# Kernel optimization log

Measured on AMD Instinct MI355X. Metric: run time of the kernel, lower is better.

The kernel has to match this reference:

```python
import jax, jax.numpy as jnp
import numpy as np

B, K, N, D, H, NNEG, NTOP = 8, 8, 128, 256, 128, 64, 64
UNARY_SCALES = (1.0, 1.0, 1.0)  # one scale per tree level, tree_height = log2(K) = 3


def setup_inputs():
    key = jax.random.key(0)
    ks = jax.random.split(key, 8)
    s = 0.05
    return {
        'pos_fea': jax.random.normal(ks[0], (B, K, N, D), jnp.float32),
        'neg_fea': jax.random.normal(ks[1], (B * K, NNEG, D), jnp.float32),
        'pos_classes': jax.random.randint(ks[2], (B, K, N), 0, 20),
        'target_class': jax.random.randint(ks[3], (B,), 0, 20),
        'Wp1': jax.random.normal(ks[4], (2 * D, H), jnp.float32) * s,
        'bp1': jnp.zeros((H,), jnp.float32),
        'Wp2': jax.random.normal(ks[5], (H, 1), jnp.float32) * s,
        'bp2': jnp.zeros((1,), jnp.float32),
        'Wu1': jax.random.normal(ks[6], (2 * D, H), jnp.float32) * s,
        'bu1': jnp.zeros((H,), jnp.float32),
        'Wu2': jax.random.normal(ks[7], (H, 1), jnp.float32) * s,
        'bu2': jnp.zeros((1,), jnp.float32),
    }


def _relation(f0, f1, W1, b1, W2, b2):
    # RelationModule: Dense(H, relu) -> Dense(1) applied to concat([f0_m, f1_n])
    # for every cross pair; concat-Dense is split into two GEMMs. -> [Bn, M0, M1]
    d = f0.shape[-1]
    h0 = jnp.einsum('bmd,dh->bmh', f0, W1[:d])
    h1 = jnp.einsum('bnd,dh->bnh', f1, W1[d:])
    h = jax.nn.relu(h0[:, :, None, :] + h1[:, None, :, :] + b1)
    return jnp.einsum('bmnh,h->bmn', h, W2[:, 0]) + b2[0]


def _bg(t, idx):
    # batched_gather along axis 1: t [Bn, P, ...], idx [Bn, T]
    ie = idx.reshape(idx.shape + (1,) * (t.ndim - 2))
    ie = jnp.broadcast_to(ie, idx.shape + t.shape[2:])
    return jnp.take_along_axis(t, ie, axis=1)


def _rep(fea, sub):
    # subproblem representative feature: fea [Bn,S,N,D], sub [Bn,M,S] -> [Bn,M,D]
    idx = jnp.swapaxes(sub, 1, 2)[..., None]              # [Bn,S,M,1]
    idx = jnp.broadcast_to(idx, idx.shape[:-1] + (fea.shape[-1],))
    return jnp.take_along_axis(fea, idx, axis=2).mean(axis=1)


def _tree(pos_fea, neg_fea, Wp1, bp1, Wp2, bp2, Wu1, bu1, Wu2, bu2):
    pos_flat = pos_fea.reshape(B * K, N, D)
    # UnaryModule: mean relation score of each positive proposal vs the negative bag
    ue = _relation(pos_flat, neg_fea, Wu1, bu1, Wu2, bu2).mean(-1)   # [B*K, N]
    sub = jnp.broadcast_to(jnp.arange(N, dtype=jnp.int32)[None, :, None], (B * K, N, 1))
    pe = jnp.zeros_like(ue)
    tree_height = int(np.log2(K))
    best = None
    for i in range(tree_height):
        S = 2 ** i                      # subproblem size per branch at this level
        Bn = sub.shape[0] // 2
        M = sub.shape[1]
        sub2 = sub.reshape(Bn, 2, M, S)  # [::2] / [1::2] split of adjacent rows
        sub0, sub1 = sub2[:, 0], sub2[:, 1]
        pe2 = pe.reshape(Bn, 2, M)
        ue2 = ue.reshape(Bn, 2, M)
        fea = pos_flat.reshape(Bn, 2, S, N, D)
        rep0 = _rep(fea[:, 0], sub0)
        rep1 = _rep(fea[:, 1], sub1)
        # PairwiseCrossSimilarity: scores for all cross pairs of candidates
        scores = _relation(rep0, rep1, Wp1, bp1, Wp2, bp2).reshape(Bn, M * M)
        p0 = jnp.repeat(jnp.arange(M), M)
        p1 = jnp.tile(jnp.arange(M), M)
        pe = pe2[:, 0][:, p0] + pe2[:, 1][:, p1] - scores
        ue = ue2[:, 0][:, p0] + ue2[:, 1][:, p1]
        total = pe + UNARY_SCALES[i] * ue
        sub = jnp.concatenate([sub0[:, p0], sub1[:, p1]], axis=-1)  # [Bn, M*M, 2S]
        topk = 1 if i == tree_height - 1 else min(M * M, NTOP)
        _, inds = jax.lax.top_k(-total, topk)
        sub = _bg(sub, inds)
        ue = jnp.take_along_axis(ue, inds, axis=1)
        pe = jnp.take_along_axis(pe, inds, axis=1)
        best = jnp.take_along_axis(total, inds, axis=1)
    return sub, best


def reference(pos_fea, neg_fea, pos_classes, target_class,
              Wp1, bp1, Wp2, bp2, Wu1, bu1, Wu2, bu2):
    sub, _ = _tree(pos_fea, neg_fea, Wp1, bp1, Wp2, bp2, Wu1, bu1, Wu2, bu2)
    is_target = (pos_classes == target_class[:, None, None]).astype(jnp.float32)
    return sub[:, 0], is_target  # selected proposal per image [B,K], [B,K,N]
```

## Files before the change

### kernel.cpp

```cpp
#include <hip/hip_runtime.h>
#include <stdint.h>

#define B_ 8
#define K_ 8
#define N_ 128
#define D_ 256
#define H_ 128
#define NNEG_ 64

typedef unsigned long long u64;
typedef float f4 __attribute__((ext_vector_type(4)));

__device__ __forceinline__ u64 shfl_xor_u64(u64 v, int m) {
    int lo = __shfl_xor((int)(unsigned)v, m, 64);
    int hi = __shfl_xor((int)(unsigned)(v >> 32), m, 64);
    return ((u64)(unsigned)hi << 32) | (unsigned)lo;
}
__device__ __forceinline__ u64 bitonic_merge64(u64 m, int lane) {
#pragma unroll
    for (int j = 32; j > 0; j >>= 1) {
        u64 o = shfl_xor_u64(m, j);
        bool keepMin = ((lane & j) == 0);
        bool lt = m < o;
        m = (keepMin == lt) ? m : o;
    }
    return m;
}
__device__ __forceinline__ u64 merge2(u64 a, u64 b, int lane) {
    u64 br = shfl_xor_u64(b, 63);
    u64 m = a < br ? a : br;
    return bitonic_merge64(m, lane);
}
__device__ __forceinline__ unsigned sortable(float f) {
    unsigned u = __float_as_uint(f);
    return (u & 0x80000000u) ? ~u : (u | 0x80000000u);
}
__device__ __forceinline__ float unsortable(unsigned u) {
    return __uint_as_float((u & 0x80000000u) ? (u & 0x7FFFFFFFu) : ~u);
}
__device__ __forceinline__ void sort128_reg(u64& v0, u64& v1, int lane) {
#pragma unroll
    for (int k = 2; k <= 64; k <<= 1) {
        bool d0 = ((lane & k) == 0);
        bool d1 = (k == 64) ? false : d0;
#pragma unroll
        for (int j = k >> 1; j > 0; j >>= 1) {
            u64 o0 = shfl_xor_u64(v0, j);
            bool km0 = (((lane & j) == 0) == d0);
            v0 = (km0 == (v0 < o0)) ? v0 : o0;
            u64 o1 = shfl_xor_u64(v1, j);
            bool km1 = (((lane & j) == 0) == d1);
            v1 = (km1 == (v1 < o1)) ? v1 : o1;
        }
    }
    if (v0 > v1) { u64 tmp = v0; v0 = v1; v1 = tmp; }
#pragma unroll
    for (int j = 32; j > 0; j >>= 1) {
        bool km = ((lane & j) == 0);
        u64 o0 = shfl_xor_u64(v0, j);
        v0 = (km == (v0 < o0)) ? v0 : o0;
        u64 o1 = shfl_xor_u64(v1, j);
        v1 = (km == (v1 < o1)) ? v1 : o1;
    }
}

__global__ __launch_bounds__(128) void g1_gemm(
    const float* __restrict__ pos, const float* __restrict__ neg,
    const float* __restrict__ Wu1, const float* __restrict__ Wp1,
    const int* __restrict__ pos_classes, const int* __restrict__ target_class,
    float* __restrict__ HU0, float* __restrict__ HU1n,
    float* __restrict__ HP0, float* __restrict__ HP1,
    float* __restrict__ outp) {
    int bid = blockIdx.x;
    int t = threadIdx.x;
    if (bid >= 896) {
        int base = (bid - 896) * 2048 + t * 16;
#pragma unroll
        for (int q = 0; q < 16; ++q) {
            int idx = base + q;
            outp[64 + idx] = (pos_classes[idx] == target_class[idx >> 10]) ? 1.0f : 0.0f;
        }
        return;
    }
    const float* A; const float* W; float* OUT; int bid2;
    if (bid < 256)      { A = pos; W = Wu1;           OUT = HU0;  bid2 = bid; }
    else if (bid < 384) { A = neg; W = Wu1 + D_ * H_; OUT = HU1n; bid2 = bid - 256; }
    else if (bid < 640) { A = pos; W = Wp1;           OUT = HP0;  bid2 = bid - 384; }
    else                { A = pos; W = Wp1 + D_ * H_; OUT = HP1;  bid2 = bid - 640; }
    int rb = (bid2 >> 1) * 64;
    int cb64 = (bid2 & 1) * 64;

    __shared__ float As[2][64][36];
    int tx = t & 7, ty = t >> 3;
    f4 acc[4][2];
#pragma unroll
    for (int i = 0; i < 4; ++i) { acc[i][0] = (f4)0.f; acc[i][1] = (f4)0.f; }

    const float* Wb = W + cb64 + tx * 8;

#pragma unroll
    for (int rep = 0; rep < 4; ++rep) {
        int flat = t + rep * 128;
        int row = flat >> 3, kq = flat & 7;
        *(f4*)&As[0][row][kq * 4] = *(const f4*)&A[(size_t)(rb + row) * D_ + kq * 4];
    }
    f4 bcur[4][2], bnxt[4][2];
#pragma unroll
    for (int q = 0; q < 4; ++q) {
        bcur[q][0] = *(const f4*)&Wb[(size_t)q * H_];
        bcur[q][1] = *(const f4*)&Wb[(size_t)q * H_ + 4];
    }
    __syncthreads();

    for (int chunk = 0; chunk < 8; ++chunk) {
        int cur = chunk & 1, nxt = cur ^ 1;
        bool pre = (chunk < 7);
        f4 pa[4];
        if (pre) {
            int k0n = (chunk + 1) * 32;
#pragma unroll
            for (int rep = 0; rep < 4; ++rep) {
                int flat = t + rep * 128;
                int row = flat >> 3, kq = flat & 7;
                pa[rep] = *(const f4*)&A[(size_t)(rb + row) * D_ + k0n + kq * 4];
            }
        }
#pragma unroll
        for (int g = 0; g < 8; ++g) {
            int kg = chunk * 8 + g;
            if (kg + 1 < 64) {
                int kb = (kg + 1) * 4;
#pragma unroll
                for (int q = 0; q < 4; ++q) {
                    bnxt[q][0] = *(const f4*)&Wb[(size_t)(kb + q) * H_];
                    bnxt[q][1] = *(const f4*)&Wb[(size_t)(kb + q) * H_ + 4];
                }
            }
            f4 av[4];
#pragma unroll
            for (int i = 0; i < 4; ++i)
                av[i] = *(const f4*)&As[cur][ty * 4 + i][g * 4];
#pragma unroll
            for (int q = 0; q < 4; ++q) {
                f4 b0 = bcur[q][0], b1 = bcur[q][1];
#pragma unroll
                for (int i = 0; i < 4; ++i) {
                    float a = av[i][q];
                    acc[i][0][0] += a * b0[0]; acc[i][0][1] += a * b0[1];
                    acc[i][0][2] += a * b0[2]; acc[i][0][3] += a * b0[3];
                    acc[i][1][0] += a * b1[0]; acc[i][1][1] += a * b1[1];
                    acc[i][1][2] += a * b1[2]; acc[i][1][3] += a * b1[3];
                }
            }
#pragma unroll
            for (int q = 0; q < 4; ++q) { bcur[q][0] = bnxt[q][0]; bcur[q][1] = bnxt[q][1]; }
        }
        if (pre) {
#pragma unroll
            for (int rep = 0; rep < 4; ++rep) {
                int flat = t + rep * 128;
                int row = flat >> 3, kq = flat & 7;
                *(f4*)&As[nxt][row][kq * 4] = pa[rep];
            }
        }
        __syncthreads();
    }
#pragma unroll
    for (int i = 0; i < 4; ++i) {
        *(f4*)&OUT[(size_t)(rb + ty * 4 + i) * H_ + cb64 + tx * 8] = acc[i][0];
        *(f4*)&OUT[(size_t)(rb + ty * 4 + i) * H_ + cb64 + tx * 8 + 4] = acc[i][1];
    }
}

__global__ __launch_bounds__(128) void g2_ue_sc0(
    const float* __restrict__ HU0, const float* __restrict__ HU1n,
    const float* __restrict__ bu1, const float* __restrict__ Wu2,
    const float* __restrict__ bu2v,
    const float* __restrict__ HP0, const float* __restrict__ HP1,
    const float* __restrict__ bp1, const float* __restrict__ Wp2,
    const float* __restrict__ bp2,
    float* __restrict__ t0, float* __restrict__ sc0) {
    __shared__ float LsT[128][36];
    __shared__ float RsT[128][68];
    __shared__ float wsv[128];
    __shared__ float red[32][33];

    int bid = blockIdx.x;
    int t = threadIdx.x;
    bool is_ue = bid < 256;

    const float* Lsrc; const float* Rsrc; const float* b1v; const float* W2;
    if (is_ue) {
        int bk = bid >> 2, mt = bid & 3;
        Lsrc = HU0 + (size_t)(bk * N_ + mt * 32) * H_;
        Rsrc = HU1n + (size_t)bk * NNEG_ * H_;
        b1v = bu1; W2 = Wu2;
    } else {
        int bid2 = bid - 256;
        int b = bid2 >> 3, m0t = (bid2 >> 1) & 3, m1t = bid2 & 1;
        Lsrc = HP0 + (size_t)b * 2 * N_ * H_ + m0t * 32 * H_;
        Rsrc = HP1 + (size_t)b * 2 * N_ * H_ + N_ * H_ + m1t * 64 * H_;
        b1v = bp1; W2 = Wp2;
    }
    for (int i = t; i < 32 * 32; i += 128) {
        int m = i & 31, hq = i >> 5;
        const f4 a = *(const f4*)&Lsrc[(size_t)m * H_ + hq * 4];
        const f4 b = *(const f4*)&b1v[hq * 4];
        LsT[hq * 4 + 0][m] = a[0] + b[0];
        LsT[hq * 4 + 1][m] = a[1] + b[1];
        LsT[hq * 4 + 2][m] = a[2] + b[2];
        LsT[hq * 4 + 3][m] = a[3] + b[3];
    }
    for (int i = t; i < 64 * 32; i += 128) {
        int n = i & 63, hq = i >> 6;
        const f4 a = *(const f4*)&Rsrc[(size_t)n * H_ + hq * 4];
        RsT[hq * 4 + 0][n] = a[0];
        RsT[hq * 4 + 1][n] = a[1];
        RsT[hq * 4 + 2][n] = a[2];
        RsT[hq * 4 + 3][n] = a[3];
    }
    wsv[t] = W2[t];
    __syncthreads();

    int tm = t & 7, tn = t >> 3;
    f4 acc[4];
#pragma unroll
    for (int i = 0; i < 4; ++i) acc[i] = (f4)0.f;
#pragma unroll 2
    for (int hg = 0; hg < 32; ++hg) {
        f4 wv = *(const f4*)&wsv[hg * 4];
        f4 lv[4], rv[4];
#pragma unroll
        for (int s = 0; s < 4; ++s) {
            lv[s] = *(const f4*)&LsT[hg * 4 + s][tm * 4];
            rv[s] = *(const f4*)&RsT[hg * 4 + s][tn * 4];
        }
#pragma unroll
        for (int s = 0; s < 4; ++s) {
            float w = wv[s];
#pragma unroll
            for (int i = 0; i < 4; ++i) {
                float l = lv[s][i];
                float v;
                v = l + rv[s][0]; v = v > 0.f ? v : 0.f; acc[i][0] += v * w;
                v = l + rv[s][1]; v = v > 0.f ? v : 0.f; acc[i][1] += v * w;
                v = l + rv[s][2]; v = v > 0.f ? v : 0.f; acc[i][2] += v * w;
                v = l + rv[s][3]; v = v > 0.f ? v : 0.f; acc[i][3] += v * w;
            }
        }
    }

    if (is_ue) {
        int bk = bid >> 2, mt = bid & 3;
#pragma unroll
        for (int i = 0; i < 4; ++i) {
            red[tm * 4 + i][tn * 2 + 0] = acc[i][0] + acc[i][1];
            red[tm * 4 + i][tn * 2 + 1] = acc[i][2] + acc[i][3];
        }
        __syncthreads();
        if (t < 32) {
            float s = 0.f;
            for (int q = 0; q < 32; ++q) s += red[t][q];
            t0[bk * N_ + mt * 32 + t] = s * (1.0f / NNEG_) + bu2v[0];
        }
    } else {
        int bid2 = bid - 256;
        int b = bid2 >> 3, m0t = (bid2 >> 1) & 3, m1t = bid2 & 1;
        float bp2v = bp2[0];
        float* orow = sc0 + (size_t)b * 16384;
#pragma unroll
        for (int i = 0; i < 4; ++i) {
            int m0 = m0t * 32 + tm * 4 + i;
            int m1 = m1t * 64 + tn * 4;
            f4 o = {acc[i][0] + bp2v, acc[i][1] + bp2v,
                    acc[i][2] + bp2v, acc[i][3] + bp2v};
            *(f4*)&orow[m0 * 128 + m1] = o;
        }
    }
}

__global__ __launch_bounds__(256) void g3a_top0(const float* __restrict__ sc0,
                                                const float* __restrict__ t0,
                                                u64* __restrict__ g3c) {
    int bid = blockIdx.x;
    int r = bid >> 3, c = bid & 7;
    int t = threadIdx.x, lane = t & 63, w = t >> 6;
    __shared__ float tt[256];
    __shared__ u64 cand[4][128];
    if (t < 256) tt[t] = t0[r * 256 + t];
    __syncthreads();
    const float* row = sc0 + (size_t)r * 16384 + c * 2048 + w * 512;
    unsigned sv[8];
#pragma unroll
    for (int j = 0; j < 8; ++j) {
        int li = j * 64 + lane;
        int idx = c * 2048 + w * 512 + li;
        float v = (tt[idx >> 7] + tt[128 + (idx & 127)]) - row[li];
        sv[j] = sortable(v);
    }
    unsigned T = 0u;
#pragma unroll
    for (int it = 0; it < 16; ++it) {
        int p = 30 - 2 * it;
        unsigned C1 = T | (1u << p), C2 = T | (2u << p), C3 = T | (3u << p);
        unsigned c1 = 0u, c2 = 0u, c3 = 0u;
#pragma unroll
        for (int j = 0; j < 8; ++j) {
            c1 += (unsigned)__popcll(__ballot(sv[j] < C1));
            c2 += (unsigned)__popcll(__ballot(sv[j] < C2));
            c3 += (unsigned)__popcll(__ballot(sv[j] < C3));
        }
        unsigned k = (c3 < 64u) ? 3u : (c2 < 64u) ? 2u : (c1 < 64u) ? 1u : 0u;
        T |= (k << p);
    }
    u64* my = cand[w];
    int base = 0;
#pragma unroll
    for (int j = 0; j < 8; ++j) {
        u64 mask = __ballot(sv[j] <= T);
        if (sv[j] <= T) {
            int pos = base + (int)__popcll(mask & ((1ull << lane) - 1ull));
            if (pos < 128) {
                int idx = c * 2048 + w * 512 + j * 64 + lane;
                my[pos] = ((u64)sv[j] << 32) | (unsigned)idx;
            }
        }
        base += (int)__popcll(mask);
    }
    int cc = base < 128 ? base : 128;
    u64 v0 = (lane < cc) ? my[lane] : ~0ull;
    u64 v1 = (64 + lane < cc) ? my[64 + lane] : ~0ull;
    sort128_reg(v0, v1, lane);
    my[lane] = v0;
    __syncthreads();
    if (w == 0) {
        u64 x0 = cand[0][lane], x1 = cand[1][lane];
        u64 x2 = cand[2][lane], x3 = cand[3][lane];
        u64 y0 = merge2(x0, x1, lane), y1 = merge2(x2, x3, lane);
        g3c[(size_t)bid * 64 + lane] = merge2(y0, y1, lane);
    }
}

__global__ __launch_bounds__(256) void g4a_s1(
    const float* __restrict__ HP0, const float* __restrict__ HP1,
    const u64* __restrict__ g3c, int* __restrict__ pA,
    const float* __restrict__ bp1, const float* __restrict__ Wp2,
    const float* __restrict__ bp2, u64* __restrict__ g4top) {
    int bid = blockIdx.x;
    int u = bid >> 3, mq = (bid >> 1) & 3, nh = bid & 1;
    int t = threadIdx.x, lane = t & 63, w = t >> 6;
    __shared__ float LsT[128][17];
    __shared__ float RsT[128][34];
    __shared__ float taL[64], taR[64];
    __shared__ int paL[64], paR[64];
    __shared__ float wsv[128];
    __shared__ u64 cand[4][64];
    if (w < 2) {
        const u64* Lp = g3c + (size_t)(2 * u + w) * 512;
        u64 x0 = Lp[lane], x1 = Lp[64 + lane], x2 = Lp[128 + lane], x3 = Lp[192 + lane];
        u64 x4 = Lp[256 + lane], x5 = Lp[320 + lane], x6 = Lp[384 + lane], x7 = Lp[448 + lane];
        u64 y0 = merge2(x0, x1, lane), y1 = merge2(x2, x3, lane);
        u64 y2 = merge2(x4, x5, lane), y3 = merge2(x6, x7, lane);
        u64 z0 = merge2(y0, y1, lane), z1 = merge2(y2, y3, lane);
        u64 f = merge2(z0, z1, lane);
        int idx = (int)(f & 0xFFFFFFFFull);
        int pk = ((idx >> 7) << 8) | (idx & 127);
        float tv = unsortable((unsigned)(f >> 32));
        if (w == 0) { taL[lane] = tv; paL[lane] = pk; }
        else        { taR[lane] = tv; paR[lane] = pk; }
    }
    if (t >= 128) wsv[t - 128] = Wp2[t - 128];
    float bp2v = bp2[0];
    __syncthreads();
    if ((bid & 7) == 0) {
        if (t < 64) pA[(2 * u) * 64 + t] = paL[t];
        else if (t < 128) pA[(2 * u + 1) * 64 + (t - 64)] = paR[t - 64];
    }
    for (int i = t; i < 16 * 128; i += 256) {
        int m = i >> 7, h = i & 127;
        int pk = paL[mq * 16 + m]; int a0 = pk >> 8, a1 = pk & 255;
        float s = HP0[(size_t)(4 * u) * 16384 + a0 * 128 + h]
                + HP0[(size_t)(4 * u + 1) * 16384 + a1 * 128 + h];
        LsT[h][m] = s * 0.5f + bp1[h];
    }
    for (int i = t; i < 32 * 128; i += 256) {
        int n = i >> 7, h = i & 127;
        int pk = paR[nh * 32 + n]; int c0 = pk >> 8, c1 = pk & 255;
        float s = HP1[(size_t)(4 * u + 2) * 16384 + c0 * 128 + h]
                + HP1[(size_t)(4 * u + 3) * 16384 + c1 * 128 + h];
        RsT[h][n] = s * 0.5f;
    }
    __syncthreads();
    int lm = w * 4 + (lane >> 4);
    int ln = lane & 15;
    float a0 = 0.f, a1 = 0.f;
#pragma unroll 4
    for (int h = 0; h < 128; ++h) {
        float lv = LsT[h][lm];
        const float2 rv = *(const float2*)&RsT[h][ln * 2];
        float wv = wsv[h];
        float v;
        v = lv + rv.x; v = v > 0.f ? v : 0.f; a0 += v * wv;
        v = lv + rv.y; v = v > 0.f ? v : 0.f; a1 += v * wv;
    }
    int m_unit = mq * 16 + lm;
    int n0 = nh * 32 + ln * 2;
    float val0 = (taL[mq * 16 + lm] + taR[nh * 32 + ln * 2 + 0]) - (a0 + bp2v);
    float val1 = (taL[mq * 16 + lm] + taR[nh * 32 + ln * 2 + 1]) - (a1 + bp2v);
    u64 v0 = ((u64)sortable(val0) << 32) | (unsigned)(m_unit * 64 + n0);
    u64 v1 = ((u64)sortable(val1) << 32) | (unsigned)(m_unit * 64 + n0 + 1);
    sort128_reg(v0, v1, lane);
    cand[w][lane] = v0;
    __syncthreads();
    if (w == 0) {
        u64 x0 = cand[0][lane], x1 = cand[1][lane];
        u64 x2 = cand[2][lane], x3 = cand[3][lane];
        u64 y0 = merge2(x0, x1, lane), y1 = merge2(x2, x3, lane);
        g4top[(size_t)bid * 64 + lane] = merge2(y0, y1, lane);
    }
}

__global__ __launch_bounds__(256) void g4b_s2(
    const float* __restrict__ HP0, const float* __restrict__ HP1,
    const int* __restrict__ pA, const u64* __restrict__ g4top,
    const float* __restrict__ bp1, const float* __restrict__ Wp2,
    const float* __restrict__ bp2, float* __restrict__ outp) {
    int b = blockIdx.x;
    int t = threadIdx.x, lane = t & 63, w = t >> 6;
    __shared__ float LsT[128][68];
    __shared__ float RsT[128][36];
    __shared__ float tL[64], tR[64];
    __shared__ unsigned subL[64], subR[64];
    __shared__ float wsv[128];
    __shared__ u64 sred[4];
    if (t < 128) wsv[t] = Wp2[t];
    float bp2v = bp2[0];
    if (w < 2) {
        const u64* Lp = g4top + (size_t)(2 * b + w) * 512;
        u64 x0 = Lp[lane], x1 = Lp[64 + lane], x2 = Lp[128 + lane], x3 = Lp[192 + lane];
        u64 x4 = Lp[256 + lane], x5 = Lp[320 + lane], x6 = Lp[384 + lane], x7 = Lp[448 + lane];
        u64 y0 = merge2(x0, x1, lane), y1 = merge2(x2, x3, lane);
        u64 y2 = merge2(x4, x5, lane), y3 = merge2(x6, x7, lane);
        u64 z0 = merge2(y0, y1, lane), z1 = merge2(y2, y3, lane);
        u64 m = merge2(z0, z1, lane);
        int idx = (int)(m & 0xFFFFFFFFull);
        int p0 = idx >> 6, p1 = idx & 63;
        float val = unsortable((unsigned)(m >> 32));
        int rowL = 4 * b + 2 * w;
        int pkL = pA[rowL * 64 + p0];
        int pkR = pA[(rowL + 1) * 64 + p1];
        unsigned leaves = ((unsigned)pkL << 16) | (unsigned)pkR;
        if (w == 0) { tL[lane] = val; subL[lane] = leaves; }
        else        { tR[lane] = val; subR[lane] = leaves; }
    }
    __syncthreads();
    for (int i = t; i < 64 * 128; i += 256) {
        int m = i >> 7, h = i & 127;
        unsigned s4 = subL[m];
        float s = HP0[(size_t)(8 * b + 0) * 16384 + ((s4 >> 24) & 255u) * 128 + h]
                + HP0[(size_t)(8 * b + 1) * 16384 + ((s4 >> 16) & 255u) * 128 + h]
                + HP0[(size_t)(8 * b + 2) * 16384 + ((s4 >> 8) & 255u) * 128 + h]
                + HP0[(size_t)(8 * b + 3) * 16384 + (s4 & 255u) * 128 + h];
        LsT[h][m] = s * 0.25f + bp1[h];
    }
    u64 best = ~0ull;
    int qm = w * 4 + (lane >> 4);
    int qn = lane & 15;
    for (int half = 0; half < 2; ++half) {
        __syncthreads();
        for (int i = t; i < 32 * 128; i += 256) {
            int n = i >> 7, h = i & 127;
            int ng = half * 32 + n;
            unsigned s4 = subR[ng];
            float s = HP1[(size_t)(8 * b + 4) * 16384 + ((s4 >> 24) & 255u) * 128 + h]
                    + HP1[(size_t)(8 * b + 5) * 16384 + ((s4 >> 16) & 255u) * 128 + h]
                    + HP1[(size_t)(8 * b + 6) * 16384 + ((s4 >> 8) & 255u) * 128 + h]
                    + HP1[(size_t)(8 * b + 7) * 16384 + (s4 & 255u) * 128 + h];
            RsT[h][n] = s * 0.25f;
        }
        __syncthreads();
        float acc[4][2];
#pragma unroll
        for (int i = 0; i < 4; ++i) { acc[i][0] = 0.f; acc[i][1] = 0.f; }
#pragma unroll 2
        for (int h = 0; h < 128; ++h) {
            const float4 lv = *(const float4*)&LsT[h][qm * 4];
            const float2 rv = *(const float2*)&RsT[h][qn * 2];
            float wv = wsv[h];
            float v;
            v = lv.x + rv.x; v = v > 0.f ? v : 0.f; acc[0][0] += v * wv;
            v = lv.x + rv.y; v = v > 0.f ? v : 0.f; acc[0][1] += v * wv;
            v = lv.y + rv.x; v = v > 0.f ? v : 0.f; acc[1][0] += v * wv;
            v = lv.y + rv.y; v = v > 0.f ? v : 0.f; acc[1][1] += v * wv;
            v = lv.z + rv.x; v = v > 0.f ? v : 0.f; acc[2][0] += v * wv;
            v = lv.z + rv.y; v = v > 0.f ? v : 0.f; acc[2][1] += v * wv;
            v = lv.w + rv.x; v = v > 0.f ? v : 0.f; acc[3][0] += v * wv;
            v = lv.w + rv.y; v = v > 0.f ? v : 0.f; acc[3][1] += v * wv;
        }
#pragma unroll
        for (int mi = 0; mi < 4; ++mi) {
#pragma unroll
            for (int nj = 0; nj < 2; ++nj) {
                int m = qm * 4 + mi;
                int ng = half * 32 + qn * 2 + nj;
                float val = (tL[m] + tR[ng]) - (acc[mi][nj] + bp2v);
                u64 kk = ((u64)sortable(val) << 32) | (unsigned)(m * 64 + ng);
                best = kk < best ? kk : best;
            }
        }
    }
#pragma unroll
    for (int off = 32; off > 0; off >>= 1) {
        u64 o = shfl_xor_u64(best, off);
        best = o < best ? o : best;
    }
    if (lane == 0) sred[w] = best;
    __syncthreads();
    if (t == 0) {
        u64 bb = sred[0];
        for (int p = 1; p < 4; ++p) { u64 o = sred[p]; bb = o < bb ? o : bb; }
        int idx = (int)(bb & 0xFFFFFFFFull);
        unsigned sl = subL[idx >> 6], sr = subR[idx & 63];
        outp[b * 8 + 0] = (float)((sl >> 24) & 255u);
        outp[b * 8 + 1] = (float)((sl >> 16) & 255u);
        outp[b * 8 + 2] = (float)((sl >> 8) & 255u);
        outp[b * 8 + 3] = (float)(sl & 255u);
        outp[b * 8 + 4] = (float)((sr >> 24) & 255u);
        outp[b * 8 + 5] = (float)((sr >> 16) & 255u);
        outp[b * 8 + 6] = (float)((sr >> 8) & 255u);
        outp[b * 8 + 7] = (float)(sr & 255u);
    }
}

extern "C" void kernel_launch(void* const* d_in, const int* in_sizes, int n_in,
                              void* d_out, int out_size, void* d_ws, size_t ws_size,
                              hipStream_t stream) {
    const float* pos = (const float*)d_in[0];
    const float* neg = (const float*)d_in[1];
    const int* pos_classes = (const int*)d_in[2];
    const int* target_class = (const int*)d_in[3];
    const float* Wp1 = (const float*)d_in[4];
    const float* bp1 = (const float*)d_in[5];
    const float* Wp2 = (const float*)d_in[6];
    const float* bp2 = (const float*)d_in[7];
    const float* Wu1 = (const float*)d_in[8];
    const float* bu1 = (const float*)d_in[9];
    const float* Wu2 = (const float*)d_in[10];
    const float* bu2 = (const float*)d_in[11];

    float* wsf = (float*)d_ws;
    float* HU0 = wsf;
    float* HP0 = HU0 + 1048576;
    float* HP1 = HP0 + 1048576;
    float* HU1n = HP1 + 1048576;
    float* t0 = HU1n + 524288;
    float* sc0 = t0 + 8192;
    int* pA = (int*)(sc0 + 524288);
    u64* g3c = (u64*)wsf;
    u64* g4top = (u64*)wsf + 16384;
    float* outp = (float*)d_out;

    g1_gemm<<<900, 128, 0, stream>>>(pos, neg, Wu1, Wp1, pos_classes,
                                     target_class, HU0, HU1n, HP0, HP1, outp);
    g2_ue_sc0<<<512, 128, 0, stream>>>(HU0, HU1n, bu1, Wu2, bu2,
                                       HP0, HP1, bp1, Wp2, bp2, t0, sc0);
    g3a_top0<<<256, 256, 0, stream>>>(sc0, t0, g3c);
    g4a_s1<<<128, 256, 0, stream>>>(HP0, HP1, g3c, pA, bp1, Wp2, bp2, g4top);
    g4b_s2<<<8, 256, 0, stream>>>(HP0, HP1, pA, g4top, bp1, Wp2, bp2, outp);
}
```

Measured before the change: 194.3 us.

## Stage GEMM weights in LDS with 8-row thread tiles; widen final-stage block

The first GEMM kernel now runs 64 threads per block. Each thread computes an 8x8 output tile, and the weight tile is staged through double-buffered shared memory instead of being read per thread from global memory. This raises per-thread arithmetic reuse and cuts redundant global weight loads, at the cost of more registers per thread and fewer waves per block. The last-level pairwise kernel moves from 256 to 512 threads and computes all 64 right-side candidates in one pass instead of two halves. That removes a loop and its barriers but doubles the shared memory used for the right-hand tile.

New measurement: 304.9 us. 1.57x slower.

```diff
diff --git a/kernel.cpp b/kernel.cpp
--- a/kernel.cpp
+++ b/kernel.cpp
@@ -64,7 +64,7 @@
     }
 }
 
-__global__ __launch_bounds__(128) void g1_gemm(
+__global__ __launch_bounds__(64) void g1_gemm(
     const float* __restrict__ pos, const float* __restrict__ neg,
     const float* __restrict__ Wu1, const float* __restrict__ Wp1,
     const int* __restrict__ pos_classes, const int* __restrict__ target_class,
@@ -74,9 +74,9 @@
     int bid = blockIdx.x;
     int t = threadIdx.x;
     if (bid >= 896) {
-        int base = (bid - 896) * 2048 + t * 16;
-#pragma unroll
-        for (int q = 0; q < 16; ++q) {
+        int base = (bid - 896) * 2048 + t * 32;
+#pragma unroll
+        for (int q = 0; q < 32; ++q) {
             int idx = base + q;
             outp[64 + idx] = (pos_classes[idx] == target_class[idx >> 10]) ? 1.0f : 0.0f;
         }
@@ -91,60 +91,57 @@
     int cb64 = (bid2 & 1) * 64;
 
     __shared__ float As[2][64][36];
+    __shared__ float Bs[2][32][64];
     int tx = t & 7, ty = t >> 3;
-    f4 acc[4][2];
-#pragma unroll
-    for (int i = 0; i < 4; ++i) { acc[i][0] = (f4)0.f; acc[i][1] = (f4)0.f; }
-
-    const float* Wb = W + cb64 + tx * 8;
-
-#pragma unroll
-    for (int rep = 0; rep < 4; ++rep) {
-        int flat = t + rep * 128;
+    f4 acc[8][2];
+#pragma unroll
+    for (int i = 0; i < 8; ++i) { acc[i][0] = (f4)0.f; acc[i][1] = (f4)0.f; }
+
+#pragma unroll
+    for (int rep = 0; rep < 8; ++rep) {
+        int flat = t + rep * 64;
         int row = flat >> 3, kq = flat & 7;
         *(f4*)&As[0][row][kq * 4] = *(const f4*)&A[(size_t)(rb + row) * D_ + kq * 4];
     }
-    f4 bcur[4][2], bnxt[4][2];
-#pragma unroll
-    for (int q = 0; q < 4; ++q) {
-        bcur[q][0] = *(const f4*)&Wb[(size_t)q * H_];
-        bcur[q][1] = *(const f4*)&Wb[(size_t)q * H_ + 4];
+#pragma unroll
+    for (int rep = 0; rep < 8; ++rep) {
+        int flat = t + rep * 64;
+        int kr = flat >> 4, cq = flat & 15;
+        *(f4*)&Bs[0][kr][cq * 4] = *(const f4*)&W[(size_t)kr * H_ + cb64 + cq * 4];
     }
     __syncthreads();
 
     for (int chunk = 0; chunk < 8; ++chunk) {
         int cur = chunk & 1, nxt = cur ^ 1;
         bool pre = (chunk < 7);
-        f4 pa[4];
+        f4 pa[8], pb[8];
         if (pre) {
             int k0n = (chunk + 1) * 32;
 #pragma unroll
-            for (int rep = 0; rep < 4; ++rep) {
-                int flat = t + rep * 128;
+            for (int rep = 0; rep < 8; ++rep) {
+                int flat = t + rep * 64;
                 int row = flat >> 3, kq = flat & 7;
                 pa[rep] = *(const f4*)&A[(size_t)(rb + row) * D_ + k0n + kq * 4];
             }
+#pragma unroll
+            for (int rep = 0; rep < 8; ++rep) {
+                int flat = t + rep * 64;
+                int kr = flat >> 4, cq = flat & 15;
+                pb[rep] = *(const f4*)&W[(size_t)(k0n + kr) * H_ + cb64 + cq * 4];
+            }
         }
 #pragma unroll
         for (int g = 0; g < 8; ++g) {
-            int kg = chunk * 8 + g;
-            if (kg + 1 < 64) {
-                int kb = (kg + 1) * 4;
-#pragma unroll
-                for (int q = 0; q < 4; ++q) {
-                    bnxt[q][0] = *(const f4*)&Wb[(size_t)(kb + q) * H_];
-                    bnxt[q][1] = *(const f4*)&Wb[(size_t)(kb + q) * H_ + 4];
-                }
-            }
-            f4 av[4];
-#pragma unroll
-            for (int i = 0; i < 4; ++i)
-                av[i] = *(const f4*)&As[cur][ty * 4 + i][g * 4];
+            f4 av[8];
+#pragma unroll
+            for (int i = 0; i < 8; ++i)
+                av[i] = *(const f4*)&As[cur][ty * 8 + i][g * 4];
 #pragma unroll
             for (int q = 0; q < 4; ++q) {
-                f4 b0 = bcur[q][0], b1 = bcur[q][1];
-#pragma unroll
-                for (int i = 0; i < 4; ++i) {
+                f4 b0 = *(const f4*)&Bs[cur][g * 4 + q][tx * 8];
+                f4 b1 = *(const f4*)&Bs[cur][g * 4 + q][tx * 8 + 4];
+#pragma unroll
+                for (int i = 0; i < 8; ++i) {
                     float a = av[i][q];
                     acc[i][0][0] += a * b0[0]; acc[i][0][1] += a * b0[1];
                     acc[i][0][2] += a * b0[2]; acc[i][0][3] += a * b0[3];
@@ -152,23 +149,27 @@
                     acc[i][1][2] += a * b1[2]; acc[i][1][3] += a * b1[3];
                 }
             }
-#pragma unroll
-            for (int q = 0; q < 4; ++q) { bcur[q][0] = bnxt[q][0]; bcur[q][1] = bnxt[q][1]; }
         }
         if (pre) {
 #pragma unroll
-            for (int rep = 0; rep < 4; ++rep) {
-                int flat = t + rep * 128;
+            for (int rep = 0; rep < 8; ++rep) {
+                int flat = t + rep * 64;
                 int row = flat >> 3, kq = flat & 7;
                 *(f4*)&As[nxt][row][kq * 4] = pa[rep];
             }
+#pragma unroll
+            for (int rep = 0; rep < 8; ++rep) {
+                int flat = t + rep * 64;
+                int kr = flat >> 4, cq = flat & 15;
+                *(f4*)&Bs[nxt][kr][cq * 4] = pb[rep];
+            }
         }
         __syncthreads();
     }
 #pragma unroll
-    for (int i = 0; i < 4; ++i) {
-        *(f4*)&OUT[(size_t)(rb + ty * 4 + i) * H_ + cb64 + tx * 8] = acc[i][0];
-        *(f4*)&OUT[(size_t)(rb + ty * 4 + i) * H_ + cb64 + tx * 8 + 4] = acc[i][1];
+    for (int i = 0; i < 8; ++i) {
+        *(f4*)&OUT[(size_t)(rb + ty * 8 + i) * H_ + cb64 + tx * 8] = acc[i][0];
+        *(f4*)&OUT[(size_t)(rb + ty * 8 + i) * H_ + cb64 + tx * 8 + 4] = acc[i][1];
     }
 }
 
@@ -420,7 +421,7 @@
     }
 }
 
-__global__ __launch_bounds__(256) void g4b_s2(
+__global__ __launch_bounds__(512) void g4b_s2(
     const float* __restrict__ HP0, const float* __restrict__ HP1,
     const int* __restrict__ pA, const u64* __restrict__ g4top,
     const float* __restrict__ bp1, const float* __restrict__ Wp2,
@@ -428,11 +429,11 @@
     int b = blockIdx.x;
     int t = threadIdx.x, lane = t & 63, w = t >> 6;
     __shared__ float LsT[128][68];
-    __shared__ float RsT[128][36];
+    __shared__ float RsT[128][68];
     __shared__ float tL[64], tR[64];
     __shared__ unsigned subL[64], subR[64];
     __shared__ float wsv[128];
-    __shared__ u64 sred[4];
+    __shared__ u64 sred[8];
     if (t < 128) wsv[t] = Wp2[t];
     float bp2v = bp2[0];
     if (w < 2) {
@@ -454,7 +455,7 @@
         else        { tR[lane] = val; subR[lane] = leaves; }
     }
     __syncthreads();
-    for (int i = t; i < 64 * 128; i += 256) {
+    for (int i = t; i < 64 * 128; i += 512) {
         int m = i >> 7, h = i & 127;
         unsigned s4 = subL[m];
         float s = HP0[(size_t)(8 * b + 0) * 16384 + ((s4 >> 24) & 255u) * 128 + h]
@@ -463,50 +464,46 @@
                 + HP0[(size_t)(8 * b + 3) * 16384 + (s4 & 255u) * 128 + h];
         LsT[h][m] = s * 0.25f + bp1[h];
     }
+    for (int i = t; i < 64 * 128; i += 512) {
+        int n = i >> 7, h = i & 127;
+        unsigned s4 = subR[n];
+        float s = HP1[(size_t)(8 * b + 4) * 16384 + ((s4 >> 24) & 255u) * 128 + h]
+                + HP1[(size_t)(8 * b + 5) * 16384 + ((s4 >> 16) & 255u) * 128 + h]
+                + HP1[(size_t)(8 * b + 6) * 16384 + ((s4 >> 8) & 255u) * 128 + h]
+                + HP1[(size_t)(8 * b + 7) * 16384 + (s4 & 255u) * 128 + h];
+        RsT[h][n] = s * 0.25f;
+    }
+    __syncthreads();
+    int qm = (w & 3) * 4 + (lane >> 4);
+    int qn = (w >> 2) * 16 + (lane & 15);
+    float acc[4][2];
+#pragma unroll
+    for (int i = 0; i < 4; ++i) { acc[i][0] = 0.f; acc[i][1] = 0.f; }
+#pragma unroll 2
+    for (int h = 0; h < 128; ++h) {
+        const float4 lv = *(const float4*)&LsT[h][qm * 4];
+        const float2 rv = *(const float2*)&RsT[h][qn * 2];
+        float wv = wsv[h];
+        float v;
+        v = lv.x + rv.x; v = v > 0.f ? v : 0.f; acc[0][0] += v * wv;
+        v = lv.x + rv.y; v = v > 0.f ? v : 0.f; acc[0][1] += v * wv;
+        v = lv.y + rv.x; v = v > 0.f ? v : 0.f; acc[1][0] += v * wv;
+        v = lv.y + rv.y; v = v > 0.f ? v : 0.f; acc[1][1] += v * wv;
+        v = lv.z + rv.x; v = v > 0.f ? v : 0.f; acc[2][0] += v * wv;
+        v = lv.z + rv.y; v = v > 0.f ? v : 0.f; acc[2][1] += v * wv;
+        v = lv.w + rv.x; v = v > 0.f ? v : 0.f; acc[3][0] += v * wv;
+        v = lv.w + rv.y; v = v > 0.f ? v : 0.f; acc[3][1] += v * wv;
+    }
     u64 best = ~0ull;
-    int qm = w * 4 + (lane >> 4);
-    int qn = lane & 15;
-    for (int half = 0; half < 2; ++half) {
-        __syncthreads();
-        for (int i = t; i < 32 * 128; i += 256) {
-            int n = i >> 7, h = i & 127;
-            int ng = half * 32 + n;
-            unsigned s4 = subR[ng];
-            float s = HP1[(size_t)(8 * b + 4) * 16384 + ((s4 >> 24) & 255u) * 128 + h]
-                    + HP1[(size_t)(8 * b + 5) * 16384 + ((s4 >> 16) & 255u) * 128 + h]
-                    + HP1[(size_t)(8 * b + 6) * 16384 + ((s4 >> 8) & 255u) * 128 + h]
-                    + HP1[(size_t)(8 * b + 7) * 16384 + (s4 & 255u) * 128 + h];
-            RsT[h][n] = s * 0.25f;
-        }
-        __syncthreads();
-        float acc[4][2];
-#pragma unroll
-        for (int i = 0; i < 4; ++i) { acc[i][0] = 0.f; acc[i][1] = 0.f; }
-#pragma unroll 2
-        for (int h = 0; h < 128; ++h) {
-            const float4 lv = *(const float4*)&LsT[h][qm * 4];
-            const float2 rv = *(const float2*)&RsT[h][qn * 2];
-            float wv = wsv[h];
-            float v;
-            v = lv.x + rv.x; v = v > 0.f ? v : 0.f; acc[0][0] += v * wv;
-            v = lv.x + rv.y; v = v > 0.f ? v : 0.f; acc[0][1] += v * wv;
-            v = lv.y + rv.x; v = v > 0.f ? v : 0.f; acc[1][0] += v * wv;
-            v = lv.y + rv.y; v = v > 0.f ? v : 0.f; acc[1][1] += v * wv;
-            v = lv.z + rv.x; v = v > 0.f ? v : 0.f; acc[2][0] += v * wv;
-            v = lv.z + rv.y; v = v > 0.f ? v : 0.f; acc[2][1] += v * wv;
-            v = lv.w + rv.x; v = v > 0.f ? v : 0.f; acc[3][0] += v * wv;
-            v = lv.w + rv.y; v = v > 0.f ? v : 0.f; acc[3][1] += v * wv;
-        }
-#pragma unroll
-        for (int mi = 0; mi < 4; ++mi) {
-#pragma unroll
-            for (int nj = 0; nj < 2; ++nj) {
-                int m = qm * 4 + mi;
-                int ng = half * 32 + qn * 2 + nj;
-                float val = (tL[m] + tR[ng]) - (acc[mi][nj] + bp2v);
-                u64 kk = ((u64)sortable(val) << 32) | (unsigned)(m * 64 + ng);
-                best = kk < best ? kk : best;
-            }
+#pragma unroll
+    for (int mi = 0; mi < 4; ++mi) {
+#pragma unroll
+        for (int nj = 0; nj < 2; ++nj) {
+            int m = qm * 4 + mi;
+            int ng = qn * 2 + nj;
+            float val = (tL[m] + tR[ng]) - (acc[mi][nj] + bp2v);
+            u64 kk = ((u64)sortable(val) << 32) | (unsigned)(m * 64 + ng);
+            best = kk < best ? kk : best;
         }
     }
 #pragma unroll
@@ -518,7 +515,7 @@
     __syncthreads();
     if (t == 0) {
         u64 bb = sred[0];
-        for (int p = 1; p < 4; ++p) { u64 o = sred[p]; bb = o < bb ? o : bb; }
+        for (int p = 1; p < 8; ++p) { u64 o = sred[p]; bb = o < bb ? o : bb; }
         int idx = (int)(bb & 0xFFFFFFFFull);
         unsigned sl = subL[idx >> 6], sr = subR[idx & 63];
         outp[b * 8 + 0] = (float)((sl >> 24) & 255u);
@@ -560,11 +557,11 @@
     u64* g4top = (u64*)wsf + 16384;
     float* outp = (float*)d_out;
 
-    g1_gemm<<<900, 128, 0, stream>>>(pos, neg, Wu1, Wp1, pos_classes,
-                                     target_class, HU0, HU1n, HP0, HP1, outp);
+    g1_gemm<<<900, 64, 0, stream>>>(pos, neg, Wu1, Wp1, pos_classes,
+                                    target_class, HU0, HU1n, HP0, HP1, outp);
     g2_ue_sc0<<<512, 128, 0, stream>>>(HU0, HU1n, bu1, Wu2, bu2,
                                        HP0, HP1, bp1, Wp2, bp2, t0, sc0);
     g3a_top0<<<256, 256, 0, stream>>>(sc0, t0, g3c);
     g4a_s1<<<128, 256, 0, stream>>>(HP0, HP1, g3c, pA, bp1, Wp2, bp2, g4top);
-    g4b_s2<<<8, 256, 0, stream>>>(HP0, HP1, pA, g4top, bp1, Wp2, bp2, outp);
-}
+    g4b_s2<<<8, 512, 0, stream>>>(HP0, HP1, pA, g4top, bp1, Wp2, bp2, outp);
+}
```
